# Optimization experiments

Hardware: AMD Instinct MI355X
Metric: run time of the kernel (lower is better)

Reference implementation:

```python
import jax, jax.numpy as jnp
import numpy as np

N, E, D, L = 100000, 400000, 300, 5
BN_EPS = 1e-5


def setup_inputs() -> dict:
    key = jax.random.key(0)
    ks = jax.random.split(key, 8)
    x = jax.random.randint(ks[0], (N, 7), 0, 5)
    edge_index = jax.random.randint(ks[1], (2, E), 0, N)
    edge_attr = jax.random.randint(ks[2], (E, 4), 0, 2)
    s = 0.1
    atom_tables = jax.random.normal(ks[3], (7, 119, D), jnp.float32) * s
    bond_tables = jax.random.normal(ks[4], (L, 4, 6, D), jnp.float32) * s
    mlp_w1 = jax.random.normal(ks[5], (L, D, 2 * D), jnp.float32) * (1.0 / np.sqrt(D))
    mlp_b1 = jnp.zeros((L, 2 * D), jnp.float32)
    mlp_w2 = jax.random.normal(ks[6], (L, 2 * D, D), jnp.float32) * (1.0 / np.sqrt(2 * D))
    mlp_b2 = jnp.zeros((L, D), jnp.float32)
    bn_gamma = jnp.ones((L, D), jnp.float32)
    bn_beta = jnp.zeros((L, D), jnp.float32)
    return dict(x=x, edge_index=edge_index, edge_attr=edge_attr,
                atom_tables=atom_tables, bond_tables=bond_tables,
                mlp_w1=mlp_w1, mlp_b1=mlp_b1, mlp_w2=mlp_w2, mlp_b2=mlp_b2,
                bn_gamma=bn_gamma, bn_beta=bn_beta)


def reference(x, edge_index, edge_attr, atom_tables, bond_tables,
              mlp_w1, mlp_b1, mlp_w2, mlp_b2, bn_gamma, bn_beta):
    n = x.shape[0]
    # add self loops (PyG add_self_loops appends them)
    loop = jnp.arange(n)
    src = jnp.concatenate([edge_index[0], loop])  # message source j
    dst = jnp.concatenate([edge_index[1], loop])  # aggregation target i
    self_loop_attr = jnp.zeros((n, 4), edge_attr.dtype).at[:, 0].set(4)
    ea = jnp.concatenate([edge_attr, self_loop_attr], axis=0)  # [E+N, 4]

    # AtomEncoder: sum of 7 per-feature embeddings -> [N, D]
    h = atom_tables[jnp.arange(7), x].sum(axis=1)

    for l in range(L):
        # BondEncoder: sum of 4 per-feature embeddings -> [E+N, D]
        e_emb = bond_tables[l][jnp.arange(4), ea].sum(axis=1)
        # GIN message = x_j + edge_emb, aggr='add' by target node
        msg = h[src] + e_emb
        agg = jax.ops.segment_sum(msg, dst, num_segments=n)
        # GIN update MLP: Linear -> ReLU -> Linear
        hid = jax.nn.relu(agg @ mlp_w1[l] + mlp_b1[l])
        out = hid @ mlp_w2[l] + mlp_b2[l]
        # BatchNorm1d (training mode: batch stats, biased var)
        mu = out.mean(axis=0)
        var = out.var(axis=0)
        out = (out - mu) / jnp.sqrt(var + BN_EPS) * bn_gamma[l] + bn_beta[l]
        # drop_ratio = 0.0 -> dropout is identity; ReLU except last layer
        if l < L - 1:
            out = jax.nn.relu(out)
        h = out
    return h  # JK='last'
```

## Files before the change

kernel.cpp:

```cpp
#include <hip/hip_runtime.h>

typedef unsigned short u16;
typedef unsigned int   u32;
typedef __bf16 bf16x8 __attribute__((ext_vector_type(8)));
typedef float  f32x4  __attribute__((ext_vector_type(4)));

__device__ __forceinline__ u16 f2bf(float f) {
    u32 u = __builtin_bit_cast(u32, f);
    u = u + 0x7fffu + ((u >> 16) & 1u);
    return (u16)(u >> 16);
}
__device__ __forceinline__ float bflo(u32 u) { return __builtin_bit_cast(float, u << 16); }
__device__ __forceinline__ float bfhi(u32 u) { return __builtin_bit_cast(float, u & 0xffff0000u); }
__device__ __forceinline__ u32 pack2(float x, float y) { return (u32)f2bf(x) | ((u32)f2bf(y) << 16); }

__device__ __forceinline__ void gll16(const u16* g, u16* l) {
    __builtin_amdgcn_global_load_lds(
        (const __attribute__((address_space(1))) void*)g,
        (__attribute__((address_space(3))) void*)l, 16, 0, 0);
}

#define NN 100000
#define EE 400000
#define DP 320
#define HP 640

__global__ void count_deg(const int* __restrict__ ei, int* __restrict__ deg, int E) {
    int e = blockIdx.x * 256 + threadIdx.x;
    if (e < E) atomicAdd(&deg[ei[E + e]], 1);
}

__global__ void scan1(const int* __restrict__ deg, int* __restrict__ out, int* __restrict__ bsums, int n) {
    __shared__ int lds[1024];
    int t = threadIdx.x;
    int i = blockIdx.x * 1024 + t;
    int v = (i < n) ? deg[i] : 0;
    lds[t] = v;
    __syncthreads();
    for (int d = 1; d < 1024; d <<= 1) {
        int add = (t >= d) ? lds[t - d] : 0;
        __syncthreads();
        lds[t] += add;
        __syncthreads();
    }
    if (i < n) out[i] = lds[t] - v;
    if (t == 1023) bsums[blockIdx.x] = lds[t];
}

__global__ void scan2(int* __restrict__ bsums, int nb) {
    __shared__ int lds[128];
    int t = threadIdx.x;
    int v = (t < nb) ? bsums[t] : 0;
    lds[t] = v;
    __syncthreads();
    for (int d = 1; d < 128; d <<= 1) {
        int add = (t >= d) ? lds[t - d] : 0;
        __syncthreads();
        lds[t] += add;
        __syncthreads();
    }
    if (t < nb) bsums[t] = lds[t] - v;
}

__global__ void scan3(int* __restrict__ out, const int* __restrict__ bsums, int n, int etot) {
    int i = blockIdx.x * 1024 + threadIdx.x;
    if (i < n) out[i] += bsums[blockIdx.x];
    else if (i == n) out[i] = etot;
}

__global__ void fill_csr(const int* __restrict__ ei, const int* __restrict__ ea,
                         int* __restrict__ cursors, u32* __restrict__ vals, int E) {
    int e = blockIdx.x * 256 + threadIdx.x;
    if (e >= E) return;
    int dst = ei[E + e];
    int src = ei[e];
    u32 code = (u32)((ea[e*4] & 1) | ((ea[e*4+1] & 1) << 1) | ((ea[e*4+2] & 1) << 2) | ((ea[e*4+3] & 1) << 3));
    int pos = atomicAdd(&cursors[dst], 1);
    vals[pos] = ((u32)src << 4) | code;
}

__global__ void conv_w1(const float* __restrict__ w, u16* __restrict__ wt) {
    int id = blockIdx.x * 256 + threadIdx.x;
    if (id >= 5 * HP * DP) return;
    int l = id / (HP * DP);
    int rem = id - l * (HP * DP);
    int n = rem / DP;
    int kidx = rem - n * DP;
    int u = kidx >> 3, e = kidx & 7;
    int kk = ((u ^ (n & 7)) << 3) | e;
    u16 v = 0;
    if (n < 600 && kk < 300) v = f2bf(w[((size_t)l * 300 + kk) * 600 + n]);
    wt[id] = v;
}
__global__ void conv_w2(const float* __restrict__ w, u16* __restrict__ wt) {
    int id = blockIdx.x * 256 + threadIdx.x;
    if (id >= 5 * DP * HP) return;
    int l = id / (DP * HP);
    int rem = id - l * (DP * HP);
    int n = rem / HP;
    int k = rem - n * HP;
    u16 v = 0;
    if (n < 300 && k < 600) v = f2bf(w[((size_t)l * 600 + k) * 300 + n]);
    wt[id] = v;
}

__global__ void atom_enc(const int* __restrict__ x, const float* __restrict__ at, u16* __restrict__ y) {
    const int i = blockIdx.x;
    const int d = threadIdx.x;
    __shared__ int xi[7];
    if (d < 7) xi[d] = x[i * 7 + d];
    __syncthreads();
    u16 v = 0;
    if (d < 300) {
        float s = 0.f;
        #pragma unroll
        for (int f = 0; f < 7; ++f) s += at[(f * 119 + xi[f]) * 300 + d];
        v = f2bf(s);
    }
    y[(size_t)i * DP + d] = v;
}

__global__ void bond_enc(const float* __restrict__ bt, float* __restrict__ emb) {
    const int c = blockIdx.x;
    const int d = threadIdx.x;
    float s = 0.f;
    if (d < 300) {
        if (c < 16) {
            #pragma unroll
            for (int f = 0; f < 4; ++f) s += bt[(f * 6 + ((c >> f) & 1)) * 300 + d];
        } else {
            s = bt[4 * 300 + d];
            #pragma unroll
            for (int f = 1; f < 4; ++f) s += bt[f * 6 * 300 + d];
        }
    }
    emb[c * DP + d] = s;
}

__global__ void bn_ss(const float* __restrict__ stats, const float* __restrict__ gamma,
                      const float* __restrict__ beta, float* __restrict__ scale,
                      float* __restrict__ shift, int n) {
    int d = threadIdx.x;
    float sc = 0.f, sh = 0.f;
    if (d < 300) {
        float inv_n = 1.0f / (float)n;
        float mu = stats[d] * inv_n;
        float var = stats[DP + d] * inv_n - mu * mu;
        float inv = 1.0f / sqrtf(var + 1e-5f);
        sc = gamma[d] * inv;
        sh = beta[d] - mu * sc;
    }
    scale[d] = sc; shift[d] = sh;
}

__global__ void bn_apply(const float* __restrict__ hraw, const float* __restrict__ scale,
                         const float* __restrict__ shift, u16* __restrict__ y) {
    const int i = blockIdx.x;
    const int d = threadIdx.x;
    float v = fmaf(scale[d], hraw[(size_t)i * DP + d], shift[d]);
    y[(size_t)i * DP + d] = f2bf(fmaxf(v, 0.f));
}

__global__ void aggregate(const u16* __restrict__ y,
                          const float* __restrict__ emb,
                          const int* __restrict__ offs, const u32* __restrict__ vals,
                          u16* __restrict__ agg, const int n) {
    const int wid = (int)((blockIdx.x * (size_t)blockDim.x + threadIdx.x) >> 6);
    const int lane = threadIdx.x & 63;
    if (wid >= n) return;
    const int j0 = lane, j1 = lane + 64, j2 = lane + 128;
    const bool has2 = (lane < 32);

    float a0x = 0.f, a0y = 0.f, a1x = 0.f, a1y = 0.f, a2x = 0.f, a2y = 0.f;

    auto accum = [&](int srcrow, const float* erow) {
        const u32* row = (const u32*)y + (size_t)srcrow * (DP / 2);
        u32 u0 = row[j0], u1 = row[j1];
        u32 u2 = has2 ? row[j2] : 0u;
        float2 e0 = *(const float2*)(erow + 2 * j0);
        float2 e1 = *(const float2*)(erow + 2 * j1);
        a0x += bflo(u0) + e0.x;  a0y += bfhi(u0) + e0.y;
        a1x += bflo(u1) + e1.x;  a1y += bfhi(u1) + e1.y;
        if (has2) {
            float2 e2 = *(const float2*)(erow + 2 * j2);
            a2x += bflo(u2) + e2.x;  a2y += bfhi(u2) + e2.y;
        }
    };

    accum(wid, emb + 16 * DP);
    const int s = offs[wid], t = offs[wid + 1];
    for (int e = s; e < t; ++e) {
        u32 v = vals[e];
        accum((int)(v >> 4), emb + (v & 15u) * DP);
    }

    u32* out = (u32*)agg + (size_t)wid * (DP / 2);
    out[j0] = pack2(a0x, a0y);
    out[j1] = pack2(a1x, a1y);
    if (has2) out[j2] = pack2(a2x, a2y);
}

__global__ __launch_bounds__(512, 4) void fused_mlp(
    const u16* __restrict__ A,
    const u16* __restrict__ W1t,
    const u16* __restrict__ W2t,
    const float* __restrict__ b1g,
    const float* __restrict__ b2g,
    float* __restrict__ H,
    float* __restrict__ st1, float* __restrict__ st2,
    const int M) {

    __shared__ __align__(16) u16 W1s[32 * 320];
    __shared__ __align__(16) u16 W2s[320 * 32];
    __shared__ __align__(16) u16 hidT[64 * 32];

    const int tid  = threadIdx.x;
    const int bm   = blockIdx.x * 64;
    const int wave = tid >> 6;
    const int lane = tid & 63;
    const int mg   = wave >> 1;
    const int ng   = wave & 1;
    const int l15  = lane & 15;
    const int q    = lane >> 4;

    for (int i = wave; i < 20; i += 8)
        gll16(W1t + (size_t)(i * 64 + lane) * 8, &W1s[i * 512]);

    bf16x8 afr[10];
    {
        int arow = bm + mg * 16 + l15;
        if (arow > M - 1) arow = M - 1;
        const u16* ap = A + (size_t)arow * DP + q * 8;
        #pragma unroll
        for (int kt = 0; kt < 10; ++kt)
            afr[kt] = __builtin_bit_cast(bf16x8, *(const uint4*)(ap + kt * 32));
    }

    f32x4 acc2[10];
    const f32x4 zero4 = {0.f, 0.f, 0.f, 0.f};
    #pragma unroll
    for (int nf = 0; nf < 10; ++nf) acc2[nf] = zero4;

    __syncthreads();

    const int rr = ng * 16 + l15;
    const int rbase = rr * 320;
    const int r7 = rr & 7;

    for (int c = 0; c < 20; ++c) {
        {
            const u16* base = W2t + c * 32;
            for (int i = wave; i < 20; i += 8) {
                int u = i * 64 + lane;
                gll16(base + (size_t)(u >> 2) * HP + (u & 3) * 8, &W2s[i * 512]);
            }
        }

        f32x4 acc1a = zero4, acc1b = zero4;
        #pragma unroll
        for (int kt = 0; kt < 10; kt += 2) {
            uint4 t0 = *(const uint4*)&W1s[rbase + ((((kt    ) * 4 + q) ^ r7) << 3)];
            uint4 t1 = *(const uint4*)&W1s[rbase + ((((kt + 1) * 4 + q) ^ r7) << 3)];
            acc1a = __builtin_amdgcn_mfma_f32_16x16x32_bf16(afr[kt],     __builtin_bit_cast(bf16x8, t0), acc1a, 0, 0, 0);
            acc1b = __builtin_amdgcn_mfma_f32_16x16x32_bf16(afr[kt + 1], __builtin_bit_cast(bf16x8, t1), acc1b, 0, 0, 0);
        }
        {
            f32x4 acc1 = acc1a + acc1b;
            int gcol = c * 32 + ng * 16 + l15;
            float bb = (gcol < 600) ? b1g[gcol] : 0.f;
            int col_in = (((ng * 2 + (l15 >> 3)) ^ q) << 3) | (l15 & 7);
            #pragma unroll
            for (int r = 0; r < 4; ++r) {
                float v = fmaxf(acc1[r] + bb, 0.f);
                hidT[(mg * 16 + q * 4 + r) * 32 + col_in] = f2bf(v);
            }
        }
        __syncthreads();

        if (c < 19) {
            const u16* base = W1t + (size_t)(c + 1) * (32 * 320);
            for (int i = wave; i < 20; i += 8)
                gll16(base + (size_t)(i * 64 + lane) * 8, &W1s[i * 512]);
        }

        bf16x8 a2;
        {
            int hrow = mg * 16 + l15;
            int gq = q ^ ((l15 >> 2) & 3);
            a2 = __builtin_bit_cast(bf16x8, *(const uint4*)&hidT[hrow * 32 + gq * 8]);
        }
        #pragma unroll
        for (int nf = 0; nf < 10; ++nf) {
            uint4 t = *(const uint4*)&W2s[(ng * 160 + nf * 16 + l15) * 32 + q * 8];
            acc2[nf] = __builtin_amdgcn_mfma_f32_16x16x32_bf16(a2, __builtin_bit_cast(bf16x8, t), acc2[nf], 0, 0, 0);
        }
        __syncthreads();
    }

    #pragma unroll
    for (int nf = 0; nf < 10; ++nf) {
        const int col = ng * 160 + nf * 16 + l15;
        const float bb = (col < 300) ? b2g[col] : 0.f;
        float s1 = 0.f, s2 = 0.f;
        #pragma unroll
        for (int r = 0; r < 4; ++r) {
            const int row = bm + mg * 16 + q * 4 + r;
            if (row < M) {
                float v = acc2[nf][r] + bb;
                H[(size_t)row * DP + col] = v;
                s1 += v; s2 += v * v;
            }
        }
        s1 += __shfl_xor(s1, 16); s1 += __shfl_xor(s1, 32);
        s2 += __shfl_xor(s2, 16); s2 += __shfl_xor(s2, 32);
        if (q == 0) { atomicAdd(&st1[col], s1); atomicAdd(&st2[col], s2); }
    }
}

__global__ void finalize(const float* __restrict__ hraw, const float* __restrict__ scale,
                         const float* __restrict__ shift, float* __restrict__ out) {
    const int i = blockIdx.x;
    const int d = threadIdx.x;
    if (d < 300) {
        float x = hraw[(size_t)i * DP + d];
        out[(size_t)i * 300 + d] = fmaf(scale[d], x, shift[d]);
    }
}

extern "C" void kernel_launch(void* const* d_in, const int* in_sizes, int n_in,
                              void* d_out, int out_size, void* d_ws, size_t ws_size,
                              hipStream_t stream) {
    const int N = NN, E = EE, L = 5;
    const int*   x     = (const int*)d_in[0];
    const int*   ei    = (const int*)d_in[1];
    const int*   ea    = (const int*)d_in[2];
    const float* at    = (const float*)d_in[3];
    const float* bt    = (const float*)d_in[4];
    const float* w1    = (const float*)d_in[5];
    const float* b1    = (const float*)d_in[6];
    const float* w2    = (const float*)d_in[7];
    const float* b2    = (const float*)d_in[8];
    const float* gamma = (const float*)d_in[9];
    const float* beta  = (const float*)d_in[10];
    float* out = (float*)d_out;

    char* ws = (char*)d_ws;
    size_t off = 0;
    auto alloc = [&](size_t bytes) { char* p = ws + off; off = (off + bytes + 255) & ~(size_t)255; return p; };
    u16* buf_y    = (u16*)alloc((size_t)N * DP * 2);
    u16* buf_agg  = (u16*)alloc((size_t)N * DP * 2);
    float* buf_h  = (float*)alloc((size_t)N * DP * 4);
    u16* w1t      = (u16*)alloc((size_t)5 * HP * DP * 2);
    u16* w2t      = (u16*)alloc((size_t)5 * DP * HP * 2);
    int* deg      = (int*)alloc((size_t)N * 4);
    int* offs     = (int*)alloc((size_t)(N + 1) * 4);
    int* cursors  = (int*)alloc((size_t)N * 4);
    u32* vals     = (u32*)alloc((size_t)E * 4);
    int* bsums    = (int*)alloc(128 * 4);
    float* emb    = (float*)alloc(17 * DP * 4);
    float* stats  = (float*)alloc(2 * DP * 4);
    float* scale  = (float*)alloc(DP * 4);
    float* shift  = (float*)alloc(DP * 4);

    (void)hipMemsetAsync(deg, 0, (size_t)N * 4, stream);
    count_deg<<<(E + 255) / 256, 256, 0, stream>>>(ei, deg, E);
    const int nb = (N + 1023) / 1024;
    scan1<<<nb, 1024, 0, stream>>>(deg, offs, bsums, N);
    scan2<<<1, 128, 0, stream>>>(bsums, nb);
    scan3<<<(N + 1 + 1023) / 1024, 1024, 0, stream>>>(offs, bsums, N, E);
    (void)hipMemcpyAsync(cursors, offs, (size_t)N * 4, hipMemcpyDeviceToDevice, stream);
    fill_csr<<<(E + 255) / 256, 256, 0, stream>>>(ei, ea, cursors, vals, E);

    conv_w1<<<(5 * HP * DP + 255) / 256, 256, 0, stream>>>(w1, w1t);
    conv_w2<<<(5 * DP * HP + 255) / 256, 256, 0, stream>>>(w2, w2t);

    atom_enc<<<N, DP, 0, stream>>>(x, at, buf_y);

    const int MB = (N + 63) / 64;
    for (int l = 0; l < L; ++l) {
        bond_enc<<<17, DP, 0, stream>>>(bt + (size_t)l * 4 * 6 * 300, emb);
        aggregate<<<(N * 64 + 255) / 256, 256, 0, stream>>>(
            buf_y, emb, offs, vals, buf_agg, N);
        (void)hipMemsetAsync(stats, 0, 2 * DP * 4, stream);
        fused_mlp<<<MB, 512, 0, stream>>>(
            buf_agg,
            w1t + (size_t)l * HP * DP, w2t + (size_t)l * DP * HP,
            b1 + (size_t)l * 600, b2 + (size_t)l * 300,
            buf_h, stats, stats + DP, N);
        bn_ss<<<1, DP, 0, stream>>>(stats, gamma + (size_t)l * 300, beta + (size_t)l * 300, scale, shift, N);
        if (l < L - 1)
            bn_apply<<<N, DP, 0, stream>>>(buf_h, scale, shift, buf_y);
    }
    finalize<<<N, DP, 0, stream>>>(buf_h, scale, shift, out);
}
```

Measured before the change: 2.178 ms.

## Double-buffer MLP weight tiles and process 128 rows per block

```diff
diff --git a/kernel.cpp b/kernel.cpp
--- a/kernel.cpp
+++ b/kernel.cpp
@@ -98,9 +98,12 @@
     int l = id / (DP * HP);
     int rem = id - l * (DP * HP);
     int n = rem / HP;
-    int k = rem - n * HP;
+    int kp = rem - n * HP;
+    int up = kp >> 3, e = kp & 7;
+    int ul = (up & ~3) | ((up & 3) ^ ((n >> 1) & 3));
+    int kk = (ul << 3) | e;
     u16 v = 0;
-    if (n < 300 && k < 600) v = f2bf(w[((size_t)l * 600 + k) * 300 + n]);
+    if (n < 300 && kk < 600) v = f2bf(w[((size_t)l * 600 + kk) * 300 + n]);
     wt[id] = v;
 }
 
@@ -200,7 +203,7 @@
     if (has2) out[j2] = pack2(a2x, a2y);
 }
 
-__global__ __launch_bounds__(512, 4) void fused_mlp(
+__global__ __launch_bounds__(512, 2) void fused_mlp(
     const u16* __restrict__ A,
     const u16* __restrict__ W1t,
     const u16* __restrict__ W2t,
@@ -210,12 +213,12 @@
     float* __restrict__ st1, float* __restrict__ st2,
     const int M) {
 
-    __shared__ __align__(16) u16 W1s[32 * 320];
-    __shared__ __align__(16) u16 W2s[320 * 32];
-    __shared__ __align__(16) u16 hidT[64 * 32];
+    __shared__ __align__(16) u16 W1s[2 * 32 * 320];
+    __shared__ __align__(16) u16 W2s[2 * 320 * 32];
+    __shared__ __align__(16) float hidF[128 * 36];
 
     const int tid  = threadIdx.x;
-    const int bm   = blockIdx.x * 64;
+    const int bm   = blockIdx.x * 128;
     const int wave = tid >> 6;
     const int lane = tid & 63;
     const int mg   = wave >> 1;
@@ -225,74 +228,99 @@
 
     for (int i = wave; i < 20; i += 8)
         gll16(W1t + (size_t)(i * 64 + lane) * 8, &W1s[i * 512]);
-
-    bf16x8 afr[10];
     {
-        int arow = bm + mg * 16 + l15;
+        const u16* g2 = W2t;
+        for (int i = wave; i < 20; i += 8) {
+            int u = i * 64 + lane;
+            gll16(g2 + (size_t)(u >> 2) * HP + (u & 3) * 8, &W2s[i * 512]);
+        }
+    }
+
+    bf16x8 afr[2][10];
+    #pragma unroll
+    for (int mf = 0; mf < 2; ++mf) {
+        int arow = bm + mg * 32 + mf * 16 + l15;
         if (arow > M - 1) arow = M - 1;
         const u16* ap = A + (size_t)arow * DP + q * 8;
         #pragma unroll
         for (int kt = 0; kt < 10; ++kt)
-            afr[kt] = __builtin_bit_cast(bf16x8, *(const uint4*)(ap + kt * 32));
-    }
-
-    f32x4 acc2[10];
+            afr[mf][kt] = __builtin_bit_cast(bf16x8, *(const uint4*)(ap + kt * 32));
+    }
+
+    f32x4 acc2[2][10];
     const f32x4 zero4 = {0.f, 0.f, 0.f, 0.f};
     #pragma unroll
-    for (int nf = 0; nf < 10; ++nf) acc2[nf] = zero4;
+    for (int mf = 0; mf < 2; ++mf)
+        #pragma unroll
+        for (int nf = 0; nf < 10; ++nf) acc2[mf][nf] = zero4;
 
     __syncthreads();
 
-    const int rr = ng * 16 + l15;
+    const int rr    = ng * 16 + l15;
     const int rbase = rr * 320;
-    const int r7 = rr & 7;
+    const int r7    = l15 & 7;
+    const int s2    = (l15 >> 1) & 3;
 
     for (int c = 0; c < 20; ++c) {
-        {
-            const u16* base = W2t + c * 32;
+        const int p = c & 1;
+        const u16* w1cur = W1s + p * 10240;
+        const u16* w2cur = W2s + p * 10240;
+
+        if (c < 19) {
+            const u16* g1 = W1t + (size_t)(c + 1) * 10240;
+            u16* l1 = W1s + (p ^ 1) * 10240;
+            for (int i = wave; i < 20; i += 8)
+                gll16(g1 + (size_t)(i * 64 + lane) * 8, l1 + i * 512);
+            const u16* g2 = W2t + (size_t)(c + 1) * 32;
+            u16* l2 = W2s + (p ^ 1) * 10240;
             for (int i = wave; i < 20; i += 8) {
                 int u = i * 64 + lane;
-                gll16(base + (size_t)(u >> 2) * HP + (u & 3) * 8, &W2s[i * 512]);
+                gll16(g2 + (size_t)(u >> 2) * HP + (u & 3) * 8, l2 + i * 512);
             }
         }
 
-        f32x4 acc1a = zero4, acc1b = zero4;
-        #pragma unroll
-        for (int kt = 0; kt < 10; kt += 2) {
-            uint4 t0 = *(const uint4*)&W1s[rbase + ((((kt    ) * 4 + q) ^ r7) << 3)];
-            uint4 t1 = *(const uint4*)&W1s[rbase + ((((kt + 1) * 4 + q) ^ r7) << 3)];
-            acc1a = __builtin_amdgcn_mfma_f32_16x16x32_bf16(afr[kt],     __builtin_bit_cast(bf16x8, t0), acc1a, 0, 0, 0);
-            acc1b = __builtin_amdgcn_mfma_f32_16x16x32_bf16(afr[kt + 1], __builtin_bit_cast(bf16x8, t1), acc1b, 0, 0, 0);
+        f32x4 acc1[2] = {zero4, zero4};
+        #pragma unroll
+        for (int kt = 0; kt < 10; ++kt) {
+            uint4 t = *(const uint4*)&w1cur[rbase + ((((kt * 4 + q)) ^ r7) << 3)];
+            bf16x8 b = __builtin_bit_cast(bf16x8, t);
+            acc1[0] = __builtin_amdgcn_mfma_f32_16x16x32_bf16(afr[0][kt], b, acc1[0], 0, 0, 0);
+            acc1[1] = __builtin_amdgcn_mfma_f32_16x16x32_bf16(afr[1][kt], b, acc1[1], 0, 0, 0);
         }
         {
-            f32x4 acc1 = acc1a + acc1b;
             int gcol = c * 32 + ng * 16 + l15;
             float bb = (gcol < 600) ? b1g[gcol] : 0.f;
-            int col_in = (((ng * 2 + (l15 >> 3)) ^ q) << 3) | (l15 & 7);
             #pragma unroll
-            for (int r = 0; r < 4; ++r) {
-                float v = fmaxf(acc1[r] + bb, 0.f);
-                hidT[(mg * 16 + q * 4 + r) * 32 + col_in] = f2bf(v);
-            }
-        }
-        __syncthreads();
-
-        if (c < 19) {
-            const u16* base = W1t + (size_t)(c + 1) * (32 * 320);
-            for (int i = wave; i < 20; i += 8)
-                gll16(base + (size_t)(i * 64 + lane) * 8, &W1s[i * 512]);
-        }
-
-        bf16x8 a2;
-        {
-            int hrow = mg * 16 + l15;
-            int gq = q ^ ((l15 >> 2) & 3);
-            a2 = __builtin_bit_cast(bf16x8, *(const uint4*)&hidT[hrow * 32 + gq * 8]);
+            for (int mf = 0; mf < 2; ++mf)
+                #pragma unroll
+                for (int r = 0; r < 4; ++r)
+                    hidF[(mg * 32 + mf * 16 + q * 4 + r) * 36 + ng * 16 + l15] =
+                        fmaxf(acc1[mf][r] + bb, 0.f);
+        }
+        asm volatile("s_waitcnt lgkmcnt(0)" ::: "memory");
+        __builtin_amdgcn_s_barrier();
+        __builtin_amdgcn_sched_barrier(0);
+
+        bf16x8 a2[2];
+        #pragma unroll
+        for (int mf = 0; mf < 2; ++mf) {
+            const float* hp = &hidF[(mg * 32 + mf * 16 + l15) * 36 + q * 8];
+            f32x4 lo = *(const f32x4*)hp;
+            f32x4 hi = *(const f32x4*)(hp + 4);
+            uint4 w;
+            w.x = pack2(lo[0], lo[1]);
+            w.y = pack2(lo[2], lo[3]);
+            w.z = pack2(hi[0], hi[1]);
+            w.w = pack2(hi[2], hi[3]);
+            a2[mf] = __builtin_bit_cast(bf16x8, w);
         }
         #pragma unroll
         for (int nf = 0; nf < 10; ++nf) {
-            uint4 t = *(const uint4*)&W2s[(ng * 160 + nf * 16 + l15) * 32 + q * 8];
-            acc2[nf] = __builtin_amdgcn_mfma_f32_16x16x32_bf16(a2, __builtin_bit_cast(bf16x8, t), acc2[nf], 0, 0, 0);
+            int row = ng * 160 + nf * 16 + l15;
+            uint4 t = *(const uint4*)&w2cur[row * 32 + ((q ^ s2) << 3)];
+            bf16x8 b = __builtin_bit_cast(bf16x8, t);
+            acc2[0][nf] = __builtin_amdgcn_mfma_f32_16x16x32_bf16(a2[0], b, acc2[0][nf], 0, 0, 0);
+            acc2[1][nf] = __builtin_amdgcn_mfma_f32_16x16x32_bf16(a2[1], b, acc2[1][nf], 0, 0, 0);
         }
         __syncthreads();
     }
@@ -301,19 +329,21 @@
     for (int nf = 0; nf < 10; ++nf) {
         const int col = ng * 160 + nf * 16 + l15;
         const float bb = (col < 300) ? b2g[col] : 0.f;
-        float s1 = 0.f, s2 = 0.f;
-        #pragma unroll
-        for (int r = 0; r < 4; ++r) {
-            const int row = bm + mg * 16 + q * 4 + r;
-            if (row < M) {
-                float v = acc2[nf][r] + bb;
-                H[(size_t)row * DP + col] = v;
-                s1 += v; s2 += v * v;
+        float s1 = 0.f, s2v = 0.f;
+        #pragma unroll
+        for (int mf = 0; mf < 2; ++mf)
+            #pragma unroll
+            for (int r = 0; r < 4; ++r) {
+                const int row = bm + mg * 32 + mf * 16 + q * 4 + r;
+                if (row < M) {
+                    float v = acc2[mf][nf][r] + bb;
+                    H[(size_t)row * DP + col] = v;
+                    s1 += v; s2v += v * v;
+                }
             }
-        }
         s1 += __shfl_xor(s1, 16); s1 += __shfl_xor(s1, 32);
-        s2 += __shfl_xor(s2, 16); s2 += __shfl_xor(s2, 32);
-        if (q == 0) { atomicAdd(&st1[col], s1); atomicAdd(&st2[col], s2); }
+        s2v += __shfl_xor(s2v, 16); s2v += __shfl_xor(s2v, 32);
+        if (q == 0) { atomicAdd(&st1[col], s1); atomicAdd(&st2[col], s2v); }
     }
 }
 
@@ -376,7 +406,7 @@
 
     atom_enc<<<N, DP, 0, stream>>>(x, at, buf_y);
 
-    const int MB = (N + 63) / 64;
+    const int MB = (N + 127) / 128;
     for (int l = 0; l < L; ++l) {
         bond_enc<<<17, DP, 0, stream>>>(bt + (size_t)l * 4 * 6 * 300, emb);
         aggregate<<<(N * 64 + 255) / 256, 256, 0, stream>>>(
```

Result: slower. 2.270 ms (+4.2%).

## Split fused MLP into two tiled double-buffered GEMMs with bf16 hidden buffer

Applied to the files above, without the earlier changes.

```diff
diff --git a/kernel.cpp b/kernel.cpp
--- a/kernel.cpp
+++ b/kernel.cpp
@@ -21,6 +21,7 @@
 }
 
 #define NN 100000
+#define MR 100096
 #define EE 400000
 #define DP 320
 #define HP 640
@@ -85,18 +86,16 @@
     int l = id / (HP * DP);
     int rem = id - l * (HP * DP);
     int n = rem / DP;
-    int kidx = rem - n * DP;
-    int u = kidx >> 3, e = kidx & 7;
-    int kk = ((u ^ (n & 7)) << 3) | e;
+    int k = rem - n * DP;
     u16 v = 0;
-    if (n < 600 && kk < 300) v = f2bf(w[((size_t)l * 300 + kk) * 600 + n]);
+    if (n < 600 && k < 300) v = f2bf(w[((size_t)l * 300 + k) * 600 + n]);
     wt[id] = v;
 }
 __global__ void conv_w2(const float* __restrict__ w, u16* __restrict__ wt) {
     int id = blockIdx.x * 256 + threadIdx.x;
-    if (id >= 5 * DP * HP) return;
-    int l = id / (DP * HP);
-    int rem = id - l * (DP * HP);
+    if (id >= 5 * 384 * HP) return;
+    int l = id / (384 * HP);
+    int rem = id - l * (384 * HP);
     int n = rem / HP;
     int k = rem - n * HP;
     u16 v = 0;
@@ -168,22 +167,21 @@
     const int wid = (int)((blockIdx.x * (size_t)blockDim.x + threadIdx.x) >> 6);
     const int lane = threadIdx.x & 63;
     if (wid >= n) return;
-    const int j0 = lane, j1 = lane + 64, j2 = lane + 128;
-    const bool has2 = (lane < 32);
-
-    float a0x = 0.f, a0y = 0.f, a1x = 0.f, a1y = 0.f, a2x = 0.f, a2y = 0.f;
+    const bool act = (lane < 40);
+
+    float acc[8];
+    #pragma unroll
+    for (int i = 0; i < 8; ++i) acc[i] = 0.f;
 
     auto accum = [&](int srcrow, const float* erow) {
-        const u32* row = (const u32*)y + (size_t)srcrow * (DP / 2);
-        u32 u0 = row[j0], u1 = row[j1];
-        u32 u2 = has2 ? row[j2] : 0u;
-        float2 e0 = *(const float2*)(erow + 2 * j0);
-        float2 e1 = *(const float2*)(erow + 2 * j1);
-        a0x += bflo(u0) + e0.x;  a0y += bfhi(u0) + e0.y;
-        a1x += bflo(u1) + e1.x;  a1y += bfhi(u1) + e1.y;
-        if (has2) {
-            float2 e2 = *(const float2*)(erow + 2 * j2);
-            a2x += bflo(u2) + e2.x;  a2y += bfhi(u2) + e2.y;
+        if (act) {
+            uint4 v = *(const uint4*)(y + (size_t)srcrow * DP + lane * 8);
+            float4 e0 = *(const float4*)(erow + lane * 8);
+            float4 e1 = *(const float4*)(erow + lane * 8 + 4);
+            acc[0] += bflo(v.x) + e0.x;  acc[1] += bfhi(v.x) + e0.y;
+            acc[2] += bflo(v.y) + e0.z;  acc[3] += bfhi(v.y) + e0.w;
+            acc[4] += bflo(v.z) + e1.x;  acc[5] += bfhi(v.z) + e1.y;
+            acc[6] += bflo(v.w) + e1.z;  acc[7] += bfhi(v.w) + e1.w;
         }
     };
 
@@ -194,126 +192,167 @@
         accum((int)(v >> 4), emb + (v & 15u) * DP);
     }
 
-    u32* out = (u32*)agg + (size_t)wid * (DP / 2);
-    out[j0] = pack2(a0x, a0y);
-    out[j1] = pack2(a1x, a1y);
-    if (has2) out[j2] = pack2(a2x, a2y);
-}
-
-__global__ __launch_bounds__(512, 4) void fused_mlp(
-    const u16* __restrict__ A,
-    const u16* __restrict__ W1t,
-    const u16* __restrict__ W2t,
-    const float* __restrict__ b1g,
-    const float* __restrict__ b2g,
-    float* __restrict__ H,
-    float* __restrict__ st1, float* __restrict__ st2,
-    const int M) {
-
-    __shared__ __align__(16) u16 W1s[32 * 320];
-    __shared__ __align__(16) u16 W2s[320 * 32];
-    __shared__ __align__(16) u16 hidT[64 * 32];
+    if (act) {
+        uint4 o;
+        o.x = pack2(acc[0], acc[1]);
+        o.y = pack2(acc[2], acc[3]);
+        o.z = pack2(acc[4], acc[5]);
+        o.w = pack2(acc[6], acc[7]);
+        *(uint4*)(agg + (size_t)wid * DP + lane * 8) = o;
+    }
+}
+
+__global__ __launch_bounds__(256, 3) void gemm1(
+    const u16* __restrict__ A, const u16* __restrict__ Bt,
+    const float* __restrict__ b1g, u16* __restrict__ hid) {
+
+    __shared__ __align__(16) u16 As[2][128 * 32];
+    __shared__ __align__(16) u16 Bs[2][128 * 32];
 
     const int tid  = threadIdx.x;
-    const int bm   = blockIdx.x * 64;
     const int wave = tid >> 6;
     const int lane = tid & 63;
-    const int mg   = wave >> 1;
-    const int ng   = wave & 1;
     const int l15  = lane & 15;
     const int q    = lane >> 4;
-
-    for (int i = wave; i < 20; i += 8)
-        gll16(W1t + (size_t)(i * 64 + lane) * 8, &W1s[i * 512]);
-
-    bf16x8 afr[10];
-    {
-        int arow = bm + mg * 16 + l15;
-        if (arow > M - 1) arow = M - 1;
-        const u16* ap = A + (size_t)arow * DP + q * 8;
-        #pragma unroll
-        for (int kt = 0; kt < 10; ++kt)
-            afr[kt] = __builtin_bit_cast(bf16x8, *(const uint4*)(ap + kt * 32));
-    }
-
-    f32x4 acc2[10];
+    const int wr   = wave >> 1, wc = wave & 1;
+    const int bn   = blockIdx.x % 5;
+    const size_t bm = (size_t)(blockIdx.x / 5) * 128;
+    const int srow = lane >> 2;
+    const int scol = (lane & 3) * 8;
+
+    f32x4 acc[4][4];
     const f32x4 zero4 = {0.f, 0.f, 0.f, 0.f};
     #pragma unroll
-    for (int nf = 0; nf < 10; ++nf) acc2[nf] = zero4;
-
+    for (int mi = 0; mi < 4; ++mi)
+        #pragma unroll
+        for (int ni = 0; ni < 4; ++ni) acc[mi][ni] = zero4;
+
+    auto stage = [&](int buf, int k0) {
+        #pragma unroll
+        for (int t = 0; t < 2; ++t) {
+            int s = wave + t * 4;
+            gll16(A + (bm + s * 16 + srow) * DP + k0 + scol, &As[buf][s * 512]);
+        }
+        #pragma unroll
+        for (int t = 0; t < 2; ++t) {
+            int s = wave + t * 4;
+            gll16(Bt + (size_t)(bn * 128 + s * 16 + srow) * DP + k0 + scol, &Bs[buf][s * 512]);
+        }
+    };
+
+    stage(0, 0);
     __syncthreads();
 
-    const int rr = ng * 16 + l15;
-    const int rbase = rr * 320;
-    const int r7 = rr & 7;
-
-    for (int c = 0; c < 20; ++c) {
-        {
-            const u16* base = W2t + c * 32;
-            for (int i = wave; i < 20; i += 8) {
-                int u = i * 64 + lane;
-                gll16(base + (size_t)(u >> 2) * HP + (u & 3) * 8, &W2s[i * 512]);
+    for (int ks = 0; ks < 10; ++ks) {
+        const int cur = ks & 1;
+        if (ks < 9) stage(cur ^ 1, (ks + 1) * 32);
+        bf16x8 af[4], bf[4];
+        #pragma unroll
+        for (int i = 0; i < 4; ++i) {
+            af[i] = __builtin_bit_cast(bf16x8, *(const uint4*)&As[cur][(wr * 64 + i * 16 + l15) * 32 + q * 8]);
+            bf[i] = __builtin_bit_cast(bf16x8, *(const uint4*)&Bs[cur][(wc * 64 + i * 16 + l15) * 32 + q * 8]);
+        }
+        #pragma unroll
+        for (int mi = 0; mi < 4; ++mi)
+            #pragma unroll
+            for (int ni = 0; ni < 4; ++ni)
+                acc[mi][ni] = __builtin_amdgcn_mfma_f32_16x16x32_bf16(af[mi], bf[ni], acc[mi][ni], 0, 0, 0);
+        __syncthreads();
+    }
+
+    #pragma unroll
+    for (int ni = 0; ni < 4; ++ni) {
+        const int col = bn * 128 + wc * 64 + ni * 16 + l15;
+        const float bb = (col < 600) ? b1g[col] : 0.f;
+        #pragma unroll
+        for (int mi = 0; mi < 4; ++mi)
+            #pragma unroll
+            for (int r = 0; r < 4; ++r) {
+                size_t row = bm + wr * 64 + mi * 16 + q * 4 + r;
+                hid[row * HP + col] = f2bf(fmaxf(acc[mi][ni][r] + bb, 0.f));
             }
-        }
-
-        f32x4 acc1a = zero4, acc1b = zero4;
-        #pragma unroll
-        for (int kt = 0; kt < 10; kt += 2) {
-            uint4 t0 = *(const uint4*)&W1s[rbase + ((((kt    ) * 4 + q) ^ r7) << 3)];
-            uint4 t1 = *(const uint4*)&W1s[rbase + ((((kt + 1) * 4 + q) ^ r7) << 3)];
-            acc1a = __builtin_amdgcn_mfma_f32_16x16x32_bf16(afr[kt],     __builtin_bit_cast(bf16x8, t0), acc1a, 0, 0, 0);
-            acc1b = __builtin_amdgcn_mfma_f32_16x16x32_bf16(afr[kt + 1], __builtin_bit_cast(bf16x8, t1), acc1b, 0, 0, 0);
-        }
-        {
-            f32x4 acc1 = acc1a + acc1b;
-            int gcol = c * 32 + ng * 16 + l15;
-            float bb = (gcol < 600) ? b1g[gcol] : 0.f;
-            int col_in = (((ng * 2 + (l15 >> 3)) ^ q) << 3) | (l15 & 7);
-            #pragma unroll
-            for (int r = 0; r < 4; ++r) {
-                float v = fmaxf(acc1[r] + bb, 0.f);
-                hidT[(mg * 16 + q * 4 + r) * 32 + col_in] = f2bf(v);
-            }
-        }
-        __syncthreads();
-
-        if (c < 19) {
-            const u16* base = W1t + (size_t)(c + 1) * (32 * 320);
-            for (int i = wave; i < 20; i += 8)
-                gll16(base + (size_t)(i * 64 + lane) * 8, &W1s[i * 512]);
-        }
-
-        bf16x8 a2;
-        {
-            int hrow = mg * 16 + l15;
-            int gq = q ^ ((l15 >> 2) & 3);
-            a2 = __builtin_bit_cast(bf16x8, *(const uint4*)&hidT[hrow * 32 + gq * 8]);
-        }
-        #pragma unroll
-        for (int nf = 0; nf < 10; ++nf) {
-            uint4 t = *(const uint4*)&W2s[(ng * 160 + nf * 16 + l15) * 32 + q * 8];
-            acc2[nf] = __builtin_amdgcn_mfma_f32_16x16x32_bf16(a2, __builtin_bit_cast(bf16x8, t), acc2[nf], 0, 0, 0);
-        }
-        __syncthreads();
-    }
-
+    }
+}
+
+__global__ __launch_bounds__(256, 3) void gemm2(
+    const u16* __restrict__ A , const u16* __restrict__ Bt ,
+    const float* __restrict__ b2g, float* __restrict__ H,
+    float* __restrict__ st1, float* __restrict__ st2, const int M) {
+
+    __shared__ __align__(16) u16 As[2][128 * 32];
+    __shared__ __align__(16) u16 Bs[2][128 * 32];
+
+    const int tid  = threadIdx.x;
+    const int wave = tid >> 6;
+    const int lane = tid & 63;
+    const int l15  = lane & 15;
+    const int q    = lane >> 4;
+    const int wr   = wave >> 1, wc = wave & 1;
+    const int bn   = blockIdx.x % 3;
+    const size_t bm = (size_t)(blockIdx.x / 3) * 128;
+    const int srow = lane >> 2;
+    const int scol = (lane & 3) * 8;
+
+    f32x4 acc[4][4];
+    const f32x4 zero4 = {0.f, 0.f, 0.f, 0.f};
     #pragma unroll
-    for (int nf = 0; nf < 10; ++nf) {
-        const int col = ng * 160 + nf * 16 + l15;
+    for (int mi = 0; mi < 4; ++mi)
+        #pragma unroll
+        for (int ni = 0; ni < 4; ++ni) acc[mi][ni] = zero4;
+
+    auto stage = [&](int buf, int k0) {
+        #pragma unroll
+        for (int t = 0; t < 2; ++t) {
+            int s = wave + t * 4;
+            gll16(A + (bm + s * 16 + srow) * HP + k0 + scol, &As[buf][s * 512]);
+        }
+        #pragma unroll
+        for (int t = 0; t < 2; ++t) {
+            int s = wave + t * 4;
+            gll16(Bt + (size_t)(bn * 128 + s * 16 + srow) * HP + k0 + scol, &Bs[buf][s * 512]);
+        }
+    };
+
+    stage(0, 0);
+    __syncthreads();
+
+    for (int ks = 0; ks < 20; ++ks) {
+        const int cur = ks & 1;
+        if (ks < 19) stage(cur ^ 1, (ks + 1) * 32);
+        bf16x8 af[4], bf[4];
+        #pragma unroll
+        for (int i = 0; i < 4; ++i) {
+            af[i] = __builtin_bit_cast(bf16x8, *(const uint4*)&As[cur][(wr * 64 + i * 16 + l15) * 32 + q * 8]);
+            bf[i] = __builtin_bit_cast(bf16x8, *(const uint4*)&Bs[cur][(wc * 64 + i * 16 + l15) * 32 + q * 8]);
+        }
+        #pragma unroll
+        for (int mi = 0; mi < 4; ++mi)
+            #pragma unroll
+            for (int ni = 0; ni < 4; ++ni)
+                acc[mi][ni] = __builtin_amdgcn_mfma_f32_16x16x32_bf16(af[mi], bf[ni], acc[mi][ni], 0, 0, 0);
+        __syncthreads();
+    }
+
+    #pragma unroll
+    for (int ni = 0; ni < 4; ++ni) {
+        const int col = bn * 128 + wc * 64 + ni * 16 + l15;
+        const bool cok = (col < DP);
         const float bb = (col < 300) ? b2g[col] : 0.f;
         float s1 = 0.f, s2 = 0.f;
         #pragma unroll
-        for (int r = 0; r < 4; ++r) {
-            const int row = bm + mg * 16 + q * 4 + r;
-            if (row < M) {
-                float v = acc2[nf][r] + bb;
-                H[(size_t)row * DP + col] = v;
-                s1 += v; s2 += v * v;
+        for (int mi = 0; mi < 4; ++mi)
+            #pragma unroll
+            for (int r = 0; r < 4; ++r) {
+                size_t row = bm + wr * 64 + mi * 16 + q * 4 + r;
+                if (cok && row < (size_t)M) {
+                    float v = acc[mi][ni][r] + bb;
+                    H[row * DP + col] = v;
+                    s1 += v; s2 += v * v;
+                }
             }
-        }
         s1 += __shfl_xor(s1, 16); s1 += __shfl_xor(s1, 32);
         s2 += __shfl_xor(s2, 16); s2 += __shfl_xor(s2, 32);
-        if (q == 0) { atomicAdd(&st1[col], s1); atomicAdd(&st2[col], s2); }
+        if (q == 0 && col < 300) { atomicAdd(&st1[col], s1); atomicAdd(&st2[col], s2); }
     }
 }
 
@@ -347,11 +386,12 @@
     char* ws = (char*)d_ws;
     size_t off = 0;
     auto alloc = [&](size_t bytes) { char* p = ws + off; off = (off + bytes + 255) & ~(size_t)255; return p; };
-    u16* buf_y    = (u16*)alloc((size_t)N * DP * 2);
-    u16* buf_agg  = (u16*)alloc((size_t)N * DP * 2);
-    float* buf_h  = (float*)alloc((size_t)N * DP * 4);
+    u16* buf_y    = (u16*)alloc((size_t)MR * DP * 2);
+    u16* buf_agg  = (u16*)alloc((size_t)MR * DP * 2);
+    u16* buf_hid  = (u16*)alloc((size_t)MR * HP * 2);
+    float* buf_h  = (float*)alloc((size_t)MR * DP * 4);
     u16* w1t      = (u16*)alloc((size_t)5 * HP * DP * 2);
-    u16* w2t      = (u16*)alloc((size_t)5 * DP * HP * 2);
+    u16* w2t      = (u16*)alloc((size_t)5 * 384 * HP * 2);
     int* deg      = (int*)alloc((size_t)N * 4);
     int* offs     = (int*)alloc((size_t)(N + 1) * 4);
     int* cursors  = (int*)alloc((size_t)N * 4);
@@ -362,6 +402,8 @@
     float* scale  = (float*)alloc(DP * 4);
     float* shift  = (float*)alloc(DP * 4);
 
+    (void)hipMemsetAsync(buf_agg + (size_t)N * DP, 0, (size_t)(MR - N) * DP * 2, stream);
+
     (void)hipMemsetAsync(deg, 0, (size_t)N * 4, stream);
     count_deg<<<(E + 255) / 256, 256, 0, stream>>>(ei, deg, E);
     const int nb = (N + 1023) / 1024;
@@ -372,20 +414,20 @@
     fill_csr<<<(E + 255) / 256, 256, 0, stream>>>(ei, ea, cursors, vals, E);
 
     conv_w1<<<(5 * HP * DP + 255) / 256, 256, 0, stream>>>(w1, w1t);
-    conv_w2<<<(5 * DP * HP + 255) / 256, 256, 0, stream>>>(w2, w2t);
+    conv_w2<<<(5 * 384 * HP + 255) / 256, 256, 0, stream>>>(w2, w2t);
 
     atom_enc<<<N, DP, 0, stream>>>(x, at, buf_y);
 
-    const int MB = (N + 63) / 64;
+    const int MB = MR / 128;
     for (int l = 0; l < L; ++l) {
         bond_enc<<<17, DP, 0, stream>>>(bt + (size_t)l * 4 * 6 * 300, emb);
         aggregate<<<(N * 64 + 255) / 256, 256, 0, stream>>>(
             buf_y, emb, offs, vals, buf_agg, N);
         (void)hipMemsetAsync(stats, 0, 2 * DP * 4, stream);
-        fused_mlp<<<MB, 512, 0, stream>>>(
-            buf_agg,
-            w1t + (size_t)l * HP * DP, w2t + (size_t)l * DP * HP,
-            b1 + (size_t)l * 600, b2 + (size_t)l * 300,
+        gemm1<<<MB * 5, 256, 0, stream>>>(
+            buf_agg, w1t + (size_t)l * HP * DP, b1 + (size_t)l * 600, buf_hid);
+        gemm2<<<MB * 3, 256, 0, stream>>>(
+            buf_hid, w2t + (size_t)l * 384 * HP, b2 + (size_t)l * 300,
             buf_h, stats, stats + DP, N);
         bn_ss<<<1, DP, 0, stream>>>(stats, gamma + (size_t)l * 300, beta + (size_t)l * 300, scale, shift, N);
         if (l < L - 1)
```

After: 2.163 ms. Within noise of the previous version (-0.7%).
